# Kernel optimization log

Hardware: AMD Instinct MI355X
Metric: run time of the kernel (lower is better)

The kernel has to match this reference:

```python
import jax, jax.numpy as jnp
import numpy as np

N_NODES = 100000
N_EDGES = 1600000
D_IN = 128
D_OUT = 128


def setup_inputs() -> dict:
    key = jax.random.key(0)
    k1, k2, k3, k4, k5 = jax.random.split(key, 5)
    x = jax.random.normal(k1, (N_NODES, D_IN), dtype=jnp.float32)
    # glorot_init: uniform in [-r, r], r = sqrt(6/(n_in+n_out))
    r = np.sqrt(6.0 / (D_IN + D_OUT))
    weight = jax.random.uniform(k2, (D_IN, D_OUT), dtype=jnp.float32, minval=-r, maxval=r)
    edge_vals = jax.random.uniform(k3, (N_EDGES,), dtype=jnp.float32)
    edge_rows = jax.random.randint(k4, (N_EDGES,), 0, N_NODES, dtype=jnp.int32)
    edge_cols = jax.random.randint(k5, (N_EDGES,), 0, N_NODES, dtype=jnp.int32)
    return {"x": x, "weight": weight, "edge_vals": edge_vals,
            "edge_rows": edge_rows, "edge_cols": edge_cols}


def reference(x, weight, edge_vals, edge_rows, edge_cols):
    # h = x @ W   [N, d_out]
    h = jnp.matmul(x, weight)
    # spmm: out[r] = sum_{edges e with row r} val_e * h[col_e]
    msg = edge_vals[:, None] * h[edge_cols]          # [E, d_out] gather
    agg = jax.ops.segment_sum(msg, edge_rows, num_segments=N_NODES)  # scatter-add
    return jax.nn.relu(agg)
```

## Files before the change

### kernel.cpp

```cpp
#include <hip/hip_runtime.h>
#include <hip/hip_bf16.h>

#define N_NODES 100000
#define N_EDGES 1600000
#define D 128
#define N_TILES 6250
#define NB 512
#define RPB 196
#define BCAP 3584
#define SB_BLKS 256
#define SB_EDGES 6250

typedef __bf16 bf16x8 __attribute__((ext_vector_type(8)));
typedef float  f32x4  __attribute__((ext_vector_type(4)));
typedef float  f32x2  __attribute__((ext_vector_type(2)));
typedef int    i32x2  __attribute__((ext_vector_type(2)));

__global__ __launch_bounds__(256) void prep_kernel(const float* __restrict__ W,
                                                   __bf16* __restrict__ WT,
                                                   int* __restrict__ bucketCnt) {
    int t = blockIdx.x * 256 + threadIdx.x;
    int k = t >> 7, n = t & 127;
    WT[n * D + k] = (__bf16)W[t];
    if (t < NB) bucketCnt[t] = 0;
}

__global__ __launch_bounds__(256) void gemm_kernel(
        const float* __restrict__ x,
        const __bf16* __restrict__ WT,
        __bf16* __restrict__ h) {
    __shared__ __bf16 lsm[4][16][144];
    const int wave = threadIdx.x >> 6;
    const int lane = threadIdx.x & 63;
    const int tile = blockIdx.x * 4 + wave;
    if (tile >= N_TILES) return;
    const int m = lane & 15, quad = lane >> 4;
    const float* xp = x + (size_t)(tile * 16 + m) * D + quad * 8;

    f32x4 acc[8];
#pragma unroll
    for (int ct = 0; ct < 8; ++ct) acc[ct] = (f32x4)(0.0f);
#pragma unroll
    for (int kk = 0; kk < 4; ++kk) {
        f32x4 a0 = *(const f32x4*)(xp + kk * 32);
        f32x4 a1 = *(const f32x4*)(xp + kk * 32 + 4);
        bf16x8 a;
#pragma unroll
        for (int j = 0; j < 4; ++j) { a[j] = (__bf16)a0[j]; a[j + 4] = (__bf16)a1[j]; }
#pragma unroll
        for (int ct = 0; ct < 8; ++ct) {
            bf16x8 b = *(const bf16x8*)(WT + (size_t)(ct * 16 + m) * D + kk * 32 + quad * 8);
            acc[ct] = __builtin_amdgcn_mfma_f32_16x16x32_bf16(a, b, acc[ct], 0, 0, 0);
        }
    }
#pragma unroll
    for (int ct = 0; ct < 8; ++ct)
#pragma unroll
        for (int r = 0; r < 4; ++r)
            lsm[wave][quad * 4 + r][ct * 16 + m] = (__bf16)acc[ct][r];
#pragma unroll
    for (int i = 0; i < 4; ++i) {
        int rl = i * 4 + quad;
        bf16x8 vv = *(const bf16x8*)&lsm[wave][rl][m * 8];
        *(bf16x8*)(h + (size_t)(tile * 16 + rl) * D + m * 8) = vv;
    }
}

__global__ __launch_bounds__(1024, 8) void scatterB_kernel(
        const int* __restrict__ rows, const int* __restrict__ cols,
        const float* __restrict__ vals,
        int* __restrict__ bucketCnt, i32x2* __restrict__ svcA) {
    __shared__ i32x2 lbuf[SB_EDGES];
    __shared__ int   lhist[NB];
    __shared__ int   sstart[NB];
    __shared__ int   lcur[NB];
    const int tid  = threadIdx.x;
    const int base = blockIdx.x * SB_EDGES;

    if (tid < NB) lhist[tid] = 0;
    __syncthreads();

    i32x2 r0, r1, r2, r3, r4, r5, r6;
    int   b0, b1, b2, b3, b4, b5, b6;
#define LOADREC(K, RK, BK)                                             \
    {                                                                  \
        int e = base + tid + (K) * 1024;                               \
        int rr = rows[e];                                              \
        BK = rr / RPB;                                                 \
        int local = rr - BK * RPB;                                     \
        RK[0] = (local << 17) | cols[e];                               \
        RK[1] = __float_as_int(vals[e]);                               \
        atomicAdd(&lhist[BK], 1);                                      \
    }
    LOADREC(0, r0, b0) LOADREC(1, r1, b1) LOADREC(2, r2, b2)
    LOADREC(3, r3, b3) LOADREC(4, r4, b4) LOADREC(5, r5, b5)
    if (tid < SB_EDGES - 6 * 1024) { LOADREC(6, r6, b6) }
#undef LOADREC
    __syncthreads();

    if (tid < 64) {
        const int bb = tid * 8;
        int run = 0;
#pragma unroll
        for (int j = 0; j < 8; ++j) run += lhist[bb + j];
        int s = run;
#pragma unroll
        for (int d = 1; d < 64; d <<= 1) {
            int t2 = __shfl_up(s, d, 64);
            if (tid >= d) s += t2;
        }
        int ex = s - run;
#pragma unroll
        for (int j = 0; j < 8; ++j) {
            sstart[bb + j] = ex;
            lcur[bb + j]   = ex;
            ex += lhist[bb + j];
        }
    }
    __syncthreads();

    lbuf[atomicAdd(&lcur[b0], 1)] = r0;
    lbuf[atomicAdd(&lcur[b1], 1)] = r1;
    lbuf[atomicAdd(&lcur[b2], 1)] = r2;
    lbuf[atomicAdd(&lcur[b3], 1)] = r3;
    lbuf[atomicAdd(&lcur[b4], 1)] = r4;
    lbuf[atomicAdd(&lcur[b5], 1)] = r5;
    if (tid < SB_EDGES - 6 * 1024) lbuf[atomicAdd(&lcur[b6], 1)] = r6;
    __syncthreads();

    if (tid < NB) {
        int n = lhist[tid];
        if (n > 0) {
            int g = atomicAdd(&bucketCnt[tid], n);
            int s = sstart[tid];
            for (int i = 0; i < n; ++i)
                if (g + i < BCAP) svcA[(size_t)tid * BCAP + g + i] = lbuf[s + i];
        }
    }
}

__device__ __forceinline__ f32x2 bf2f(unsigned u) {
    f32x2 r;
    r[0] = __int_as_float(u << 16);
    r[1] = __int_as_float(u & 0xffff0000u);
    return r;
}

__global__ __launch_bounds__(1024, 8) void sortsum_kernel(
        const __bf16* __restrict__ h, const int* __restrict__ bucketCnt,
        const i32x2* __restrict__ svcA, float* __restrict__ out) {
    __shared__ i32x2 lbuf[BCAP];
    __shared__ int   lhist[256];
    __shared__ int   send[256];
    __shared__ int   lcur[256];
    const int b   = blockIdx.x;
    const int tid = threadIdx.x;
    const int n   = min(bucketCnt[b], BCAP);
    const i32x2* win = svcA + (size_t)b * BCAP;

    if (tid < 256) lhist[tid] = 0;
    __syncthreads();

    i32x2 rec0, rec1, rec2, rec3;
    const int i0 = tid, i1 = tid + 1024, i2 = tid + 2048, i3 = tid + 3072;
    if (i0 < n) { rec0 = win[i0]; atomicAdd(&lhist[((unsigned)rec0[0]) >> 17], 1); }
    if (i1 < n) { rec1 = win[i1]; atomicAdd(&lhist[((unsigned)rec1[0]) >> 17], 1); }
    if (i2 < n) { rec2 = win[i2]; atomicAdd(&lhist[((unsigned)rec2[0]) >> 17], 1); }
    if (i3 < n) { rec3 = win[i3]; atomicAdd(&lhist[((unsigned)rec3[0]) >> 17], 1); }
    __syncthreads();

    if (tid < 64) {
        int b0 = lhist[tid * 4 + 0], b1 = lhist[tid * 4 + 1];
        int b2 = lhist[tid * 4 + 2], b3 = lhist[tid * 4 + 3];
        int p0 = b0, p1 = p0 + b1, p2 = p1 + b2, p3 = p2 + b3;
        int s = p3;
#pragma unroll
        for (int d = 1; d < 64; d <<= 1) {
            int t2 = __shfl_up(s, d, 64);
            if (tid >= d) s += t2;
        }
        int ex = s - p3;
        send[tid * 4 + 0] = ex + p0;
        send[tid * 4 + 1] = ex + p1;
        send[tid * 4 + 2] = ex + p2;
        send[tid * 4 + 3] = ex + p3;
        lcur[tid * 4 + 0] = ex;
        lcur[tid * 4 + 1] = ex + p0;
        lcur[tid * 4 + 2] = ex + p1;
        lcur[tid * 4 + 3] = ex + p2;
    }
    __syncthreads();

    if (i0 < n) { int rl = ((unsigned)rec0[0]) >> 17; lbuf[atomicAdd(&lcur[rl], 1)] = rec0; }
    if (i1 < n) { int rl = ((unsigned)rec1[0]) >> 17; lbuf[atomicAdd(&lcur[rl], 1)] = rec1; }
    if (i2 < n) { int rl = ((unsigned)rec2[0]) >> 17; lbuf[atomicAdd(&lcur[rl], 1)] = rec2; }
    if (i3 < n) { int rl = ((unsigned)rec3[0]) >> 17; lbuf[atomicAdd(&lcur[rl], 1)] = rec3; }
    __syncthreads();

    const int wave = tid >> 6;
    const int lane = tid & 63;
    const char* hb = (const char*)h;
    const unsigned lo4 = (unsigned)lane * 4u;
    for (int rl = wave; rl < RPB; rl += 16) {
        int gr = b * RPB + rl;
        if (gr >= N_NODES) break;
        int s = rl ? send[rl - 1] : 0;
        int e = send[rl];

        f32x2 acc0 = (f32x2)(0.0f), acc1 = (f32x2)(0.0f);
        f32x2 acc2 = (f32x2)(0.0f), acc3 = (f32x2)(0.0f);
        int i = s;
        for (; i + 7 < e; i += 8) {
            i32x2 r0 = lbuf[i],     r1 = lbuf[i + 1], r2 = lbuf[i + 2], r3 = lbuf[i + 3];
            i32x2 r4 = lbuf[i + 4], r5 = lbuf[i + 5], r6 = lbuf[i + 6], r7 = lbuf[i + 7];
            unsigned o0 = (((unsigned)r0[0] & 0x1FFFFu) << 8) + lo4;
            unsigned o1 = (((unsigned)r1[0] & 0x1FFFFu) << 8) + lo4;
            unsigned o2 = (((unsigned)r2[0] & 0x1FFFFu) << 8) + lo4;
            unsigned o3 = (((unsigned)r3[0] & 0x1FFFFu) << 8) + lo4;
            unsigned o4 = (((unsigned)r4[0] & 0x1FFFFu) << 8) + lo4;
            unsigned o5 = (((unsigned)r5[0] & 0x1FFFFu) << 8) + lo4;
            unsigned o6 = (((unsigned)r6[0] & 0x1FFFFu) << 8) + lo4;
            unsigned o7 = (((unsigned)r7[0] & 0x1FFFFu) << 8) + lo4;
            unsigned u0 = *(const unsigned*)(hb + o0);
            unsigned u1 = *(const unsigned*)(hb + o1);
            unsigned u2 = *(const unsigned*)(hb + o2);
            unsigned u3 = *(const unsigned*)(hb + o3);
            unsigned u4 = *(const unsigned*)(hb + o4);
            unsigned u5 = *(const unsigned*)(hb + o5);
            unsigned u6 = *(const unsigned*)(hb + o6);
            unsigned u7 = *(const unsigned*)(hb + o7);
            acc0 += bf2f(u0) * __int_as_float(r0[1]);
            acc1 += bf2f(u1) * __int_as_float(r1[1]);
            acc2 += bf2f(u2) * __int_as_float(r2[1]);
            acc3 += bf2f(u3) * __int_as_float(r3[1]);
            acc0 += bf2f(u4) * __int_as_float(r4[1]);
            acc1 += bf2f(u5) * __int_as_float(r5[1]);
            acc2 += bf2f(u6) * __int_as_float(r6[1]);
            acc3 += bf2f(u7) * __int_as_float(r7[1]);
        }
        for (; i + 3 < e; i += 4) {
            i32x2 r0 = lbuf[i], r1 = lbuf[i + 1], r2 = lbuf[i + 2], r3 = lbuf[i + 3];
            unsigned o0 = (((unsigned)r0[0] & 0x1FFFFu) << 8) + lo4;
            unsigned o1 = (((unsigned)r1[0] & 0x1FFFFu) << 8) + lo4;
            unsigned o2 = (((unsigned)r2[0] & 0x1FFFFu) << 8) + lo4;
            unsigned o3 = (((unsigned)r3[0] & 0x1FFFFu) << 8) + lo4;
            unsigned u0 = *(const unsigned*)(hb + o0);
            unsigned u1 = *(const unsigned*)(hb + o1);
            unsigned u2 = *(const unsigned*)(hb + o2);
            unsigned u3 = *(const unsigned*)(hb + o3);
            acc0 += bf2f(u0) * __int_as_float(r0[1]);
            acc1 += bf2f(u1) * __int_as_float(r1[1]);
            acc2 += bf2f(u2) * __int_as_float(r2[1]);
            acc3 += bf2f(u3) * __int_as_float(r3[1]);
        }
        for (; i < e; ++i) {
            i32x2 r0 = lbuf[i];
            unsigned o0 = (((unsigned)r0[0] & 0x1FFFFu) << 8) + lo4;
            unsigned u0 = *(const unsigned*)(hb + o0);
            acc0 += bf2f(u0) * __int_as_float(r0[1]);
        }

        f32x2 t01 = acc0 + acc1, t23 = acc2 + acc3;
        f32x2 tt = t01 + t23;
        f32x2 o;
        o[0] = fmaxf(tt[0], 0.0f);
        o[1] = fmaxf(tt[1], 0.0f);
        __builtin_nontemporal_store(o, (f32x2*)(out + (size_t)gr * D + lane * 2));
    }
}

extern "C" void kernel_launch(void* const* d_in, const int* in_sizes, int n_in,
                              void* d_out, int out_size, void* d_ws, size_t ws_size,
                              hipStream_t stream) {
    const float* x    = (const float*)d_in[0];
    const float* w    = (const float*)d_in[1];
    const float* vals = (const float*)d_in[2];
    const int*   rows = (const int*)d_in[3];
    const int*   cols = (const int*)d_in[4];
    float*       out  = (float*)d_out;

    char* p = (char*)d_ws;
    __bf16* h         = (__bf16*)p;  p += (size_t)N_NODES * D * 2;
    __bf16* WT        = (__bf16*)p;  p += (size_t)D * D * 2;
    int*    bucketCnt = (int*)p;     p += 4096;
    i32x2*  svcA      = (i32x2*)p;   p += (size_t)NB * BCAP * 8;

    prep_kernel<<<64, 256, 0, stream>>>(w, WT, bucketCnt);
    gemm_kernel<<<(N_TILES + 3) / 4, 256, 0, stream>>>(x, WT, h);
    scatterB_kernel<<<SB_BLKS, 1024, 0, stream>>>(rows, cols, vals, bucketCnt, svcA);
    sortsum_kernel<<<NB, 1024, 0, stream>>>(h, bucketCnt, svcA, out);
}
```

Baseline: 220.4 us.

## Fuse prep, GEMM, bucket scatter and segment-sum into one cooperative kernel

Replaces the four separate launches with a single cooperative mega-kernel of 512 blocks of 1024 threads, separated by two grid-wide syncs. Phase one bins edges locally and transposes W; phase two flushes the bins to global buckets and runs the bf16 MFMA GEMM; phase three does the per-bucket sort and gather-sum with ReLU. The aim is to cut launch gaps and tail idle time between kernels. The cost is grid-sync overhead and a co-residency requirement of two large blocks per CU; if the cooperative launch fails, the code falls back to the old four-kernel path.

```diff
diff --git a/kernel.cpp b/kernel.cpp
--- a/kernel.cpp
+++ b/kernel.cpp
@@ -1,5 +1,8 @@
 #include <hip/hip_runtime.h>
 #include <hip/hip_bf16.h>
+#include <hip/hip_cooperative_groups.h>
+
+namespace cg = cooperative_groups;
 
 #define N_NODES 100000
 #define N_EDGES 1600000
@@ -8,6 +11,8 @@
 #define NB 512
 #define RPB 196
 #define BCAP 3584
+#define MG_BLKS 512
+#define MG_EDGES 3125
 #define SB_BLKS 256
 #define SB_EDGES 6250
 
@@ -15,6 +20,261 @@
 typedef float  f32x4  __attribute__((ext_vector_type(4)));
 typedef float  f32x2  __attribute__((ext_vector_type(2)));
 typedef int    i32x2  __attribute__((ext_vector_type(2)));
+
+__device__ __forceinline__ f32x2 bf2f(unsigned u) {
+    f32x2 r;
+    r[0] = __int_as_float(u << 16);
+    r[1] = __int_as_float(u & 0xffff0000u);
+    return r;
+}
+
+__global__ __launch_bounds__(1024, 8) void mega_kernel(
+        const float* __restrict__ x, const float* __restrict__ W,
+        const float* __restrict__ vals, const int* __restrict__ rows,
+        const int* __restrict__ cols, float* __restrict__ out,
+        __bf16* __restrict__ h, __bf16* __restrict__ WT,
+        int* __restrict__ bucketCnt, i32x2* __restrict__ svcA) {
+    __shared__ __align__(16) char smem[73728];
+    const int tid = threadIdx.x;
+    const int bid = blockIdx.x;
+    cg::grid_group grid = cg::this_grid();
+
+    {
+        i32x2* lbuf  = (i32x2*)smem;
+        int* lhist   = (int*)(smem + 25000);
+        int* sstart  = (int*)(smem + 27048);
+        int* lcur    = (int*)(smem + 29096);
+        if (tid < NB) lhist[tid] = 0;
+        __syncthreads();
+
+        const int base = bid * MG_EDGES;
+        i32x2 r0, r1, r2, r3;
+        int   b0, b1, b2, b3;
+#define LOADREC(K, RK, BK)                                             \
+        {                                                              \
+            int e = base + tid + (K) * 1024;                           \
+            int rr = rows[e];                                          \
+            BK = rr / RPB;                                             \
+            int local = rr - BK * RPB;                                 \
+            RK[0] = (local << 17) | cols[e];                           \
+            RK[1] = __float_as_int(vals[e]);                           \
+            atomicAdd(&lhist[BK], 1);                                  \
+        }
+        LOADREC(0, r0, b0) LOADREC(1, r1, b1) LOADREC(2, r2, b2)
+        if (tid < MG_EDGES - 3 * 1024) { LOADREC(3, r3, b3) }
+#undef LOADREC
+
+        if (bid < 16) {
+            int t = bid * 1024 + tid;
+            int k = t >> 7, n2 = t & 127;
+            WT[n2 * D + k] = (__bf16)W[t];
+        }
+        if (bid == 16 && tid < NB) bucketCnt[tid] = 0;
+        __syncthreads();
+
+        if (tid < 64) {
+            const int bb = tid * 8;
+            int run = 0;
+#pragma unroll
+            for (int j = 0; j < 8; ++j) run += lhist[bb + j];
+            int s = run;
+#pragma unroll
+            for (int d = 1; d < 64; d <<= 1) {
+                int t2 = __shfl_up(s, d, 64);
+                if (tid >= d) s += t2;
+            }
+            int ex = s - run;
+#pragma unroll
+            for (int j = 0; j < 8; ++j) {
+                sstart[bb + j] = ex;
+                lcur[bb + j]   = ex;
+                ex += lhist[bb + j];
+            }
+        }
+        __syncthreads();
+
+        lbuf[atomicAdd(&lcur[b0], 1)] = r0;
+        lbuf[atomicAdd(&lcur[b1], 1)] = r1;
+        lbuf[atomicAdd(&lcur[b2], 1)] = r2;
+        if (tid < MG_EDGES - 3 * 1024) lbuf[atomicAdd(&lcur[b3], 1)] = r3;
+        __syncthreads();
+    }
+    grid.sync();
+
+    {
+        i32x2* lbuf  = (i32x2*)smem;
+        int* lhist   = (int*)(smem + 25000);
+        int* sstart  = (int*)(smem + 27048);
+        if (tid < NB) {
+            int n = lhist[tid];
+            if (n > 0) {
+                int g = atomicAdd(&bucketCnt[tid], n);
+                int s = sstart[tid];
+                for (int i = 0; i < n; ++i)
+                    if (g + i < BCAP) svcA[(size_t)tid * BCAP + g + i] = lbuf[s + i];
+            }
+        }
+        __syncthreads();
+
+        const int wave = tid >> 6;
+        const int lane = tid & 63;
+        const int tile = bid * 16 + wave;
+        if (tile < N_TILES) {
+            __bf16 (*lsm)[144] = (__bf16 (*)[144])(smem + wave * 4608);
+            const int m = lane & 15, quad = lane >> 4;
+            const float* xp = x + (size_t)(tile * 16 + m) * D + quad * 8;
+
+            f32x4 acc[8];
+#pragma unroll
+            for (int ct = 0; ct < 8; ++ct) acc[ct] = (f32x4)(0.0f);
+#pragma unroll
+            for (int kk = 0; kk < 4; ++kk) {
+                f32x4 a0 = *(const f32x4*)(xp + kk * 32);
+                f32x4 a1 = *(const f32x4*)(xp + kk * 32 + 4);
+                bf16x8 a;
+#pragma unroll
+                for (int j = 0; j < 4; ++j) { a[j] = (__bf16)a0[j]; a[j + 4] = (__bf16)a1[j]; }
+#pragma unroll
+                for (int ct = 0; ct < 8; ++ct) {
+                    bf16x8 bfrag = *(const bf16x8*)(WT + (size_t)(ct * 16 + m) * D + kk * 32 + quad * 8);
+                    acc[ct] = __builtin_amdgcn_mfma_f32_16x16x32_bf16(a, bfrag, acc[ct], 0, 0, 0);
+                }
+            }
+#pragma unroll
+            for (int ct = 0; ct < 8; ++ct)
+#pragma unroll
+                for (int r = 0; r < 4; ++r)
+                    lsm[quad * 4 + r][ct * 16 + m] = (__bf16)acc[ct][r];
+#pragma unroll
+            for (int i = 0; i < 4; ++i) {
+                int rl = i * 4 + quad;
+                bf16x8 vv = *(const bf16x8*)&lsm[rl][m * 8];
+                *(bf16x8*)(h + (size_t)(tile * 16 + rl) * D + m * 8) = vv;
+            }
+        }
+    }
+    grid.sync();
+
+    {
+        i32x2* lbuf = (i32x2*)smem;
+        int* lhist  = (int*)(smem + 28672);
+        int* send   = (int*)(smem + 29696);
+        int* lcur   = (int*)(smem + 30720);
+        const int b = bid;
+        const int n = min(bucketCnt[b], BCAP);
+        const i32x2* win = svcA + (size_t)b * BCAP;
+
+        if (tid < 256) lhist[tid] = 0;
+        __syncthreads();
+
+        i32x2 rec0, rec1, rec2, rec3;
+        const int i0 = tid, i1 = tid + 1024, i2 = tid + 2048, i3 = tid + 3072;
+        if (i0 < n) { rec0 = win[i0]; atomicAdd(&lhist[((unsigned)rec0[0]) >> 17], 1); }
+        if (i1 < n) { rec1 = win[i1]; atomicAdd(&lhist[((unsigned)rec1[0]) >> 17], 1); }
+        if (i2 < n) { rec2 = win[i2]; atomicAdd(&lhist[((unsigned)rec2[0]) >> 17], 1); }
+        if (i3 < n) { rec3 = win[i3]; atomicAdd(&lhist[((unsigned)rec3[0]) >> 17], 1); }
+        __syncthreads();
+
+        if (tid < 64) {
+            int b0 = lhist[tid * 4 + 0], b1 = lhist[tid * 4 + 1];
+            int b2 = lhist[tid * 4 + 2], b3 = lhist[tid * 4 + 3];
+            int p0 = b0, p1 = p0 + b1, p2 = p1 + b2, p3 = p2 + b3;
+            int s = p3;
+#pragma unroll
+            for (int d = 1; d < 64; d <<= 1) {
+                int t2 = __shfl_up(s, d, 64);
+                if (tid >= d) s += t2;
+            }
+            int ex = s - p3;
+            send[tid * 4 + 0] = ex + p0;
+            send[tid * 4 + 1] = ex + p1;
+            send[tid * 4 + 2] = ex + p2;
+            send[tid * 4 + 3] = ex + p3;
+            lcur[tid * 4 + 0] = ex;
+            lcur[tid * 4 + 1] = ex + p0;
+            lcur[tid * 4 + 2] = ex + p1;
+            lcur[tid * 4 + 3] = ex + p2;
+        }
+        __syncthreads();
+
+        if (i0 < n) { int rl = ((unsigned)rec0[0]) >> 17; lbuf[atomicAdd(&lcur[rl], 1)] = rec0; }
+        if (i1 < n) { int rl = ((unsigned)rec1[0]) >> 17; lbuf[atomicAdd(&lcur[rl], 1)] = rec1; }
+        if (i2 < n) { int rl = ((unsigned)rec2[0]) >> 17; lbuf[atomicAdd(&lcur[rl], 1)] = rec2; }
+        if (i3 < n) { int rl = ((unsigned)rec3[0]) >> 17; lbuf[atomicAdd(&lcur[rl], 1)] = rec3; }
+        __syncthreads();
+
+        const int wave = tid >> 6;
+        const int lane = tid & 63;
+        const char* hb = (const char*)h;
+        const unsigned lo4 = (unsigned)lane * 4u;
+        for (int rl = wave; rl < RPB; rl += 16) {
+            int gr = b * RPB + rl;
+            if (gr >= N_NODES) break;
+            int s = rl ? send[rl - 1] : 0;
+            int e = send[rl];
+
+            f32x2 acc0 = (f32x2)(0.0f), acc1 = (f32x2)(0.0f);
+            f32x2 acc2 = (f32x2)(0.0f), acc3 = (f32x2)(0.0f);
+            int i = s;
+            for (; i + 7 < e; i += 8) {
+                i32x2 r0 = lbuf[i],     r1 = lbuf[i + 1], r2 = lbuf[i + 2], r3 = lbuf[i + 3];
+                i32x2 r4 = lbuf[i + 4], r5 = lbuf[i + 5], r6 = lbuf[i + 6], r7 = lbuf[i + 7];
+                unsigned o0 = (((unsigned)r0[0] & 0x1FFFFu) << 8) + lo4;
+                unsigned o1 = (((unsigned)r1[0] & 0x1FFFFu) << 8) + lo4;
+                unsigned o2 = (((unsigned)r2[0] & 0x1FFFFu) << 8) + lo4;
+                unsigned o3 = (((unsigned)r3[0] & 0x1FFFFu) << 8) + lo4;
+                unsigned o4 = (((unsigned)r4[0] & 0x1FFFFu) << 8) + lo4;
+                unsigned o5 = (((unsigned)r5[0] & 0x1FFFFu) << 8) + lo4;
+                unsigned o6 = (((unsigned)r6[0] & 0x1FFFFu) << 8) + lo4;
+                unsigned o7 = (((unsigned)r7[0] & 0x1FFFFu) << 8) + lo4;
+                unsigned u0 = *(const unsigned*)(hb + o0);
+                unsigned u1 = *(const unsigned*)(hb + o1);
+                unsigned u2 = *(const unsigned*)(hb + o2);
+                unsigned u3 = *(const unsigned*)(hb + o3);
+                unsigned u4 = *(const unsigned*)(hb + o4);
+                unsigned u5 = *(const unsigned*)(hb + o5);
+                unsigned u6 = *(const unsigned*)(hb + o6);
+                unsigned u7 = *(const unsigned*)(hb + o7);
+                acc0 += bf2f(u0) * __int_as_float(r0[1]);
+                acc1 += bf2f(u1) * __int_as_float(r1[1]);
+                acc2 += bf2f(u2) * __int_as_float(r2[1]);
+                acc3 += bf2f(u3) * __int_as_float(r3[1]);
+                acc0 += bf2f(u4) * __int_as_float(r4[1]);
+                acc1 += bf2f(u5) * __int_as_float(r5[1]);
+                acc2 += bf2f(u6) * __int_as_float(r6[1]);
+                acc3 += bf2f(u7) * __int_as_float(r7[1]);
+            }
+            for (; i + 3 < e; i += 4) {
+                i32x2 r0 = lbuf[i], r1 = lbuf[i + 1], r2 = lbuf[i + 2], r3 = lbuf[i + 3];
+                unsigned o0 = (((unsigned)r0[0] & 0x1FFFFu) << 8) + lo4;
+                unsigned o1 = (((unsigned)r1[0] & 0x1FFFFu) << 8) + lo4;
+                unsigned o2 = (((unsigned)r2[0] & 0x1FFFFu) << 8) + lo4;
+                unsigned o3 = (((unsigned)r3[0] & 0x1FFFFu) << 8) + lo4;
+                unsigned u0 = *(const unsigned*)(hb + o0);
+                unsigned u1 = *(const unsigned*)(hb + o1);
+                unsigned u2 = *(const unsigned*)(hb + o2);
+                unsigned u3 = *(const unsigned*)(hb + o3);
+                acc0 += bf2f(u0) * __int_as_float(r0[1]);
+                acc1 += bf2f(u1) * __int_as_float(r1[1]);
+                acc2 += bf2f(u2) * __int_as_float(r2[1]);
+                acc3 += bf2f(u3) * __int_as_float(r3[1]);
+            }
+            for (; i < e; ++i) {
+                i32x2 r0 = lbuf[i];
+                unsigned o0 = (((unsigned)r0[0] & 0x1FFFFu) << 8) + lo4;
+                unsigned u0 = *(const unsigned*)(hb + o0);
+                acc0 += bf2f(u0) * __int_as_float(r0[1]);
+            }
+
+            f32x2 t01 = acc0 + acc1, t23 = acc2 + acc3;
+            f32x2 tt = t01 + t23;
+            f32x2 o;
+            o[0] = fmaxf(tt[0], 0.0f);
+            o[1] = fmaxf(tt[1], 0.0f);
+            __builtin_nontemporal_store(o, (f32x2*)(out + (size_t)gr * D + lane * 2));
+        }
+    }
+}
 
 __global__ __launch_bounds__(256) void prep_kernel(const float* __restrict__ W,
                                                    __bf16* __restrict__ WT,
@@ -137,13 +397,6 @@
                 if (g + i < BCAP) svcA[(size_t)tid * BCAP + g + i] = lbuf[s + i];
         }
     }
-}
-
-__device__ __forceinline__ f32x2 bf2f(unsigned u) {
-    f32x2 r;
-    r[0] = __int_as_float(u << 16);
-    r[1] = __int_as_float(u & 0xffff0000u);
-    return r;
 }
 
 __global__ __launch_bounds__(1024, 8) void sortsum_kernel(
@@ -285,8 +538,16 @@
     int*    bucketCnt = (int*)p;     p += 4096;
     i32x2*  svcA      = (i32x2*)p;   p += (size_t)NB * BCAP * 8;
 
-    prep_kernel<<<64, 256, 0, stream>>>(w, WT, bucketCnt);
-    gemm_kernel<<<(N_TILES + 3) / 4, 256, 0, stream>>>(x, WT, h);
-    scatterB_kernel<<<SB_BLKS, 1024, 0, stream>>>(rows, cols, vals, bucketCnt, svcA);
-    sortsum_kernel<<<NB, 1024, 0, stream>>>(h, bucketCnt, svcA, out);
-}
+    void* kargs[] = {(void*)&x, (void*)&w, (void*)&vals, (void*)&rows, (void*)&cols,
+                     (void*)&out, (void*)&h, (void*)&WT, (void*)&bucketCnt, (void*)&svcA};
+    hipError_t err = hipLaunchCooperativeKernel((const void*)mega_kernel,
+                                                dim3(MG_BLKS), dim3(1024),
+                                                kargs, 0, stream);
+    if (err != hipSuccess) {
+        (void)hipGetLastError();
+        prep_kernel<<<64, 256, 0, stream>>>(w, WT, bucketCnt);
+        gemm_kernel<<<(N_TILES + 3) / 4, 256, 0, stream>>>(x, WT, h);
+        scatterB_kernel<<<SB_BLKS, 1024, 0, stream>>>(rows, cols, vals, bucketCnt, svcA);
+        sortsum_kernel<<<NB, 1024, 0, stream>>>(h, bucketCnt, svcA, out);
+    }
+}
```

New measurement: 333.0 us. 51.0% more time.
